# Kernel optimization log

Measured on AMD Instinct MI355X. Metric: run time of the kernel, lower is better.

The kernel has to match this reference:

```python
import jax, jax.numpy as jnp
import numpy as np
from jax import lax

B, L = 8, 128
V, P = 30000, 50
EMB, POS = 300, 30
H = 256            # rnn_hidden per direction
H2 = 2 * H         # BiLSTM output dim
NBIO, NLAB = 9, 10
ROUNDS = 2
IN = EMB + POS
NEG = -100000000000.0


def setup_inputs() -> dict:
    key = jax.random.key(0)
    ks = jax.random.split(key, 25)
    tokens = jax.random.randint(ks[0], (B, L), 1, V)
    pos = jax.random.randint(ks[1], (B, L), 1, P)
    lens = jax.random.randint(ks[2], (B,), L // 2, L + 1)
    mask_s = (jnp.arange(L)[None, :] < lens[:, None]).astype(jnp.float32)

    def g(k, shape, s=0.05):
        return jax.random.normal(k, shape, dtype=jnp.float32) * s

    return dict(
        tokens=tokens, pos=pos, mask_s=mask_s,
        emb=g(ks[3], (V, EMB), 0.5), pos_emb=g(ks[4], (P, POS), 0.5),
        Wih_f=g(ks[5], (4 * H, IN)), Whh_f=g(ks[6], (4 * H, H)), b_f=g(ks[7], (4 * H,)),
        Wih_b=g(ks[8], (4 * H, IN)), Whh_b=g(ks[9], (4 * H, H)), b_b=g(ks[10], (4 * H,)),
        Wg_ih=g(ks[11], (3 * H2, NBIO)), Wg_hh=g(ks[12], (3 * H2, H2)),
        bg_ih=g(ks[13], (3 * H2,)), bg_hh=g(ks[14], (3 * H2,)),
        Wr_ih=g(ks[15], (3 * H2, NLAB)), Wr_hh=g(ks[16], (3 * H2, H2)),
        br_ih=g(ks[17], (3 * H2,)), br_hh=g(ks[18], (3 * H2,)),
        W_Lr=g(ks[19], (H2, 2 * H2)), b_Lr=g(ks[20], (H2,)),
        W_Cr=g(ks[21], (NLAB, H2)), b_Cr=g(ks[22], (NLAB,)),
        W_Cg=g(ks[23], (NBIO, H2)), b_Cg=g(ks[24], (NBIO,)),
    )


def lstm_dir(x, m, Wih, Whh, b, reverse):
    # x: [B,L,IN], m: [B,L]. Masked updates emulate pack_padded_sequence
    # (state held at padded steps; padded outputs zeroed by caller).
    Bn = x.shape[0]
    h0 = jnp.zeros((Bn, H), x.dtype)
    c0 = jnp.zeros((Bn, H), x.dtype)

    def step(carry, inp):
        h, c = carry
        xt, mt = inp  # [B,IN], [B,1]
        gates = xt @ Wih.T + h @ Whh.T + b
        i, f, g, o = jnp.split(gates, 4, axis=-1)
        i = jax.nn.sigmoid(i); f = jax.nn.sigmoid(f)
        g = jnp.tanh(g); o = jax.nn.sigmoid(o)
        c_new = f * c + i * g
        h_new = o * jnp.tanh(c_new)
        h = mt * h_new + (1.0 - mt) * h
        c = mt * c_new + (1.0 - mt) * c
        return (h, c), h

    xs = (jnp.swapaxes(x, 0, 1), m.T[:, :, None])
    _, hs = lax.scan(step, (h0, c0), xs, reverse=reverse)
    return jnp.swapaxes(hs, 0, 1)  # [B,L,H]


def gru_cell(x, h, Wih, Whh, bih, bhh):
    gi = x @ Wih.T + bih
    gh = h @ Whh.T + bhh
    ir, iz, inn = jnp.split(gi, 3, axis=-1)
    hr, hz, hn = jnp.split(gh, 3, axis=-1)
    r = jax.nn.sigmoid(ir + hr)
    z = jax.nn.sigmoid(iz + hz)
    n = jnp.tanh(inn + r * hn)
    return (1.0 - z) * n + z * h


def pair_scores(Hr, W_Lr, b_Lr, W_Cr, b_Cr):
    # Lr([e1;e2]) split: e12 @ W_Lr.T = e1 @ W1.T + e2 @ W2.T (avoids 4H concat)
    W1, W2 = W_Lr[:, :H2], W_Lr[:, H2:]
    a = jnp.einsum('blh,oh->blo', Hr, W1)  # [B,L,H2]
    b2 = jnp.einsum('blh,oh->blo', Hr, W2)
    e = jax.nn.relu(a[:, :, None, :] + b2[:, None, :, :] + b_Lr)  # [B,L,L,H2]
    return jax.nn.sigmoid(jnp.einsum('bsth,kh->bstk', e, W_Cr) + b_Cr)  # [B,L,L,NLAB]


def reference(tokens, pos, mask_s, emb, pos_emb,
              Wih_f, Whh_f, b_f, Wih_b, Whh_b, b_b,
              Wg_ih, Wg_hh, bg_ih, bg_hh,
              Wr_ih, Wr_hh, br_ih, br_hh,
              W_Lr, b_Lr, W_Cr, b_Cr, W_Cg, b_Cg):
    x = jnp.concatenate([emb[tokens], pos_emb[pos]], axis=2)  # [B,L,IN]
    hf = lstm_dir(x, mask_s, Wih_f, Whh_f, b_f, reverse=False)
    hb = lstm_dir(x, mask_s, Wih_b, Whh_b, b_b, reverse=True)
    Henc = jnp.concatenate([hf, hb], axis=2) * mask_s[:, :, None]  # [B,L,H2]

    m2 = mask_s[:, :, None] * mask_s[:, None, :]  # [B,L,L] pair mask
    m3 = m2[:, :, :, None]                        # [B,L,L,1]

    Hc, Hg, Hr = Henc, Henc, Henc
    for _ in range(ROUNDS):
        prob_Cg = jax.nn.softmax(Hg @ W_Cg.T + b_Cg, axis=2)        # [B,L,NBIO]
        prob_Cr = pair_scores(Hr, W_Lr, b_Lr, W_Cr, b_Cr)            # [B,L,L,NLAB]
        prob_Cr = jnp.where(m3 > 0, prob_Cr, NEG)
        prob_Cr = prob_Cr.max(axis=2)                                # [B,L,NLAB]
        hflat = Hc.reshape(-1, H2)
        Hg = gru_cell(prob_Cg.reshape(-1, NBIO), hflat, Wg_ih, Wg_hh, bg_ih, bg_hh).reshape(Hc.shape)
        Hr = gru_cell(prob_Cr.reshape(-1, NLAB), hflat, Wr_ih, Wr_hh, br_ih, br_hh).reshape(Hc.shape)
        Hc = Hc + Hr + Hg

    logits_Cg = jax.nn.log_softmax(Hg @ W_Cg.T + b_Cg, axis=2) * mask_s[:, :, None]
    logits_Cr = pair_scores(Hr, W_Lr, b_Lr, W_Cr, b_Cr) * m3
    return logits_Cg, logits_Cr
```

## Files before the change

### kernel.cpp

```cpp
#include <hip/hip_runtime.h>
#include <hip/hip_bf16.h>
#include <stdint.h>

#define DEVI __device__ __forceinline__

static constexpr int Bn = 8, Ln = 128;
static constexpr int EMBc = 300, POSc = 30, INc = 330;
static constexpr int KPAD = 384;
static constexpr int Hc = 256, H2c = 512, G4 = 1024, G3 = 1536;
static constexpr int G2 = 2048;
static constexpr int GHW = 3072;
static constexpr int NBIOc = 9, NLABc = 10;
static constexpr float NEGc = -100000000000.0f;

typedef __attribute__((ext_vector_type(8))) short bf16x8;
typedef __attribute__((ext_vector_type(4))) float f32x4;

DEVI float sigf(float x) { return 1.0f / (1.0f + __expf(-x)); }

DEVI unsigned short b16rne(float f) {
    union { float f; unsigned u; } v; v.f = f;
    unsigned u = v.u;
    return (unsigned short)((u + 0x7FFFu + ((u >> 16) & 1u)) >> 16);
}

__global__ void k_prep0(const int* __restrict__ tok, const int* __restrict__ pos,
                        const float* __restrict__ emb, const float* __restrict__ pemb,
                        const float* __restrict__ WihF, const float* __restrict__ WihB,
                        const float* __restrict__ bF, const float* __restrict__ bB,
                        ushort* __restrict__ x, ushort* __restrict__ WihFB,
                        float* __restrict__ biasFB, uint32_t* __restrict__ hG32) {
    int i = blockIdx.x * 256 + threadIdx.x;
    const int N0 = Bn * Ln * KPAD;
    const int N1 = N0 + G2 * KPAD;
    const int N2 = N1 + G2;
    const int N3 = N2 + 8192;
    if (i < N0) {
        int bl = i / KPAD, c = i - bl * KPAD;
        float v = 0.f;
        if (c < EMBc) v = emb[tok[bl] * EMBc + c];
        else if (c < INc) v = pemb[pos[bl] * POSc + (c - EMBc)];
        x[i] = b16rne(v);
    } else if (i < N1) {
        int w = i - N0;
        int r = w / KPAD, c = w - r * KPAD;
        float v = 0.f;
        if (c < INc) v = (r < G4) ? WihF[(size_t)r * INc + c] : WihB[(size_t)(r - G4) * INc + c];
        WihFB[w] = b16rne(v);
    } else if (i < N2) {
        int j = i - N1;
        biasFB[j] = (j < G4) ? bF[j] : bB[j - G4];
    } else if (i < N3) {
        __hip_atomic_store(&hG32[i - N2], 0u, __ATOMIC_RELAXED, __HIP_MEMORY_SCOPE_AGENT);
    }
}

DEVI void gemm_tile(const ushort* __restrict__ A, const ushort* __restrict__ B,
                    const float* __restrict__ bias, float* __restrict__ C,
                    int N, int K, int m0, int n0,
                    ushort (*As)[72], ushort (*Bs)[72]) {
    int tid = threadIdx.x;
    int lane = tid & 63, wv = tid >> 6;
    int mw = (wv >> 1) * 32, nw = (wv & 1) * 32;
    int lr16 = lane & 15, g4 = lane >> 4;
    f32x4 acc[2][2] = {};
    for (int k0 = 0; k0 < K; k0 += 64) {
#pragma unroll
        for (int it = 0; it < 2; it++) {
            int idx = tid + it * 256;
            int r = idx >> 3, ch = idx & 7;
            uint4 av = *(const uint4*)(A + (size_t)(m0 + r) * K + k0 + ch * 8);
            *(uint4*)(&As[r][ch * 8]) = av;
            uint4 bv2 = *(const uint4*)(B + (size_t)(n0 + r) * K + k0 + ch * 8);
            *(uint4*)(&Bs[r][ch * 8]) = bv2;
        }
        __syncthreads();
#pragma unroll
        for (int ks = 0; ks < 2; ks++) {
            bf16x8 af[2], bfr[2];
#pragma unroll
            for (int i = 0; i < 2; i++) {
                af[i]  = *(const bf16x8*)(&As[mw + i * 16 + lr16][ks * 32 + g4 * 8]);
                bfr[i] = *(const bf16x8*)(&Bs[nw + i * 16 + lr16][ks * 32 + g4 * 8]);
            }
#pragma unroll
            for (int i = 0; i < 2; i++)
#pragma unroll
                for (int j = 0; j < 2; j++)
                    acc[i][j] = __builtin_amdgcn_mfma_f32_16x16x32_bf16(af[i], bfr[j], acc[i][j], 0, 0, 0);
        }
        __syncthreads();
    }
#pragma unroll
    for (int i = 0; i < 2; i++)
#pragma unroll
        for (int j = 0; j < 2; j++)
#pragma unroll
            for (int r2 = 0; r2 < 4; r2++) {
                int mm = m0 + mw + i * 16 + g4 * 4 + r2;
                int nn = n0 + nw + j * 16 + lr16;
                C[(size_t)mm * N + nn] = acc[i][j][r2] + (bias ? bias[nn] : 0.f);
            }
}

__global__ __launch_bounds__(256) void k_xproj(
    const ushort* __restrict__ x_bf, const ushort* __restrict__ WihFB,
    const float* __restrict__ biasFB, float* __restrict__ Xpre,
    const float* __restrict__ Wg_hh, const float* __restrict__ Wr_hh,
    const float* __restrict__ W_Lr, const float* __restrict__ bg_hh,
    const float* __restrict__ br_hh,
    const float* __restrict__ Wg_ih, const float* __restrict__ Wr_ih,
    ushort* __restrict__ WhhGR, ushort* __restrict__ WLrAB, float* __restrict__ biasGR,
    float* __restrict__ WgihT, float* __restrict__ WrihT) {
    int bid = blockIdx.x;
    __shared__ __align__(16) ushort As[64][72];
    __shared__ __align__(16) ushort Bs[64][72];
    if (bid < 512) {
        int nt = bid & 31, mt = bid >> 5;
        gemm_tile(x_bf, WihFB, biasFB, Xpre, G2, KPAD, mt * 64, nt * 64, As, Bs);
        return;
    }
    const int stride = 128 * 256;
    int pid = (bid - 512) * 256 + threadIdx.x;
    for (int idx = pid; idx < GHW * H2c; idx += stride) {
        int r = idx >> 9, c = idx & 511;
        float v = (r < G3) ? Wg_hh[(size_t)r * H2c + c] : Wr_hh[(size_t)(r - G3) * H2c + c];
        WhhGR[idx] = b16rne(v);
    }
    for (int idx = pid; idx < G4 * H2c; idx += stride) {
        int r = idx >> 9, c = idx & 511;
        float v = (r < H2c) ? W_Lr[(size_t)r * (2 * H2c) + c]
                            : W_Lr[(size_t)(r - H2c) * (2 * H2c) + H2c + c];
        WLrAB[idx] = b16rne(v);
    }
    for (int idx = pid; idx < GHW; idx += stride)
        biasGR[idx] = (idx < G3) ? bg_hh[idx] : br_hh[idx - G3];
    for (int idx = pid; idx < NBIOc * G3; idx += stride) {
        int k = idx / G3, rj = idx - k * G3;
        WgihT[idx] = Wg_ih[(size_t)rj * NBIOc + k];
    }
    for (int idx = pid; idx < NLABc * G3; idx += stride) {
        int k = idx / G3, rj = idx - k * G3;
        WrihT[idx] = Wr_ih[(size_t)rj * NLABc + k];
    }
}

__global__ __launch_bounds__(512) void k_lstm_mfma(
    const float* __restrict__ Xpre, const float* __restrict__ WhhF,
    const float* __restrict__ WhhB, const float* __restrict__ mask,
    float* __restrict__ Henc, ushort* __restrict__ HencB,
    unsigned long long* __restrict__ hG) {
    const int blk = blockIdx.x;
    const int d = blk >> 2, q = blk & 3;
    const float* Whh = d ? WhhB : WhhF;
    const int tid = threadIdx.x;
    const int lane = tid & 63, wv = tid >> 6;
    const int lr16 = lane & 15, g4 = lane >> 4;

    __shared__ __align__(16) uint32_t hlds[2][8 * 136];
    __shared__ float Glds[256][9];

    bf16x8 aw[16];
#pragma unroll
    for (int jt2 = 0; jt2 < 2; jt2++) {
        int jt = wv * 2 + jt2;
        int lr = jt * 16 + lr16;
        int g = lr >> 6, jj = lr & 63;
        int R = g * 256 + q * 64 + jj;
        const float* wr = Whh + (size_t)R * 256;
#pragma unroll
        for (int kt = 0; kt < 8; kt++) {
            int k0 = kt * 32 + g4 * 8;
            float4 f0 = *(const float4*)(wr + k0);
            float4 f1 = *(const float4*)(wr + k0 + 4);
            bf16x8 a;
            a[0] = (short)b16rne(f0.x); a[1] = (short)b16rne(f0.y);
            a[2] = (short)b16rne(f0.z); a[3] = (short)b16rne(f0.w);
            a[4] = (short)b16rne(f1.x); a[5] = (short)b16rne(f1.y);
            a[6] = (short)b16rne(f1.z); a[7] = (short)b16rne(f1.w);
            aw[jt2 * 8 + kt] = a;
        }
    }

    const int jj_t = tid & 63, b_t = tid >> 6;
    float hval = 0.f, cval = 0.f;
    const int bcol = lane & 15;
    const int bb = lane & 7;
    const int u1 = tid + 512;

    for (int s = 0; s < Ln; s++) {
        const int t = d ? (Ln - 1 - s) : s;

        const float* xrow = Xpre + ((size_t)(b_t * Ln + t)) * G2 + d * G4 + q * 64 + jj_t;
        float xg0 = xrow[0], xg1 = xrow[256], xg2 = xrow[512], xg3 = xrow[768];
        float mval = mask[b_t * Ln + t];

        const unsigned long long* slot = hG + ((size_t)(s & 1) * 2 + d) * 1024;
        unsigned long long ea, eb;
        do {
            ea = __hip_atomic_load(slot + tid, __ATOMIC_RELAXED, __HIP_MEMORY_SCOPE_AGENT);
            eb = __hip_atomic_load(slot + u1,  __ATOMIC_RELAXED, __HIP_MEMORY_SCOPE_AGENT);
        } while ((unsigned)(ea >> 32) != (unsigned)s || (unsigned)(eb >> 32) != (unsigned)s);
        uint32_t* hb = hlds[s & 1];
        hb[(tid >> 7) * 136 + (tid & 127)] = (uint32_t)ea;
        hb[(u1 >> 7) * 136 + (u1 & 127)]  = (uint32_t)eb;
        __syncthreads();

        bf16x8 bv[8];
#pragma unroll
        for (int kt = 0; kt < 8; kt++)
            bv[kt] = *(const bf16x8*)(&hb[bb * 136 + kt * 16 + g4 * 4]);

        f32x4 acc0 = {0.f, 0.f, 0.f, 0.f}, acc1 = {0.f, 0.f, 0.f, 0.f};
#pragma unroll
        for (int kt = 0; kt < 8; kt++) {
            acc0 = __builtin_amdgcn_mfma_f32_16x16x32_bf16(aw[kt], bv[kt], acc0, 0, 0, 0);
            acc1 = __builtin_amdgcn_mfma_f32_16x16x32_bf16(aw[8 + kt], bv[kt], acc1, 0, 0, 0);
        }

        if (bcol < 8) {
            int lrb0 = (wv * 2 + 0) * 16 + g4 * 4;
            int lrb1 = (wv * 2 + 1) * 16 + g4 * 4;
#pragma unroll
            for (int r2 = 0; r2 < 4; r2++) Glds[lrb0 + r2][bcol] = acc0[r2];
#pragma unroll
            for (int r2 = 0; r2 < 4; r2++) Glds[lrb1 + r2][bcol] = acc1[r2];
        }
        __syncthreads();

        float iv = sigf(xg0 + Glds[jj_t][b_t]);
        float fv = sigf(xg1 + Glds[64 + jj_t][b_t]);
        float gv = tanhf(xg2 + Glds[128 + jj_t][b_t]);
        float ov = sigf(xg3 + Glds[192 + jj_t][b_t]);
        float cn = fv * cval + iv * gv;
        float hn = ov * tanhf(cn);
        float hv = mval * hn + (1.f - mval) * hval;
        cval = mval * cn + (1.f - mval) * cval;
        hval = hv;

        int hbits = (int)b16rne(hv);
        int pbits = __shfl_xor(hbits, 1);
        if ((jj_t & 1) == 0) {
            uint32_t dataw = ((uint32_t)hbits & 0xFFFFu) | ((uint32_t)pbits << 16);
            unsigned long long word = ((unsigned long long)(unsigned)(s + 1) << 32) | dataw;
            __hip_atomic_store(hG + ((size_t)((s + 1) & 1) * 2 + d) * 1024 +
                                   b_t * 128 + q * 32 + (jj_t >> 1),
                               word, __ATOMIC_RELAXED, __HIP_MEMORY_SCOPE_AGENT);
        }
        float ho = hv * mval;
        size_t hidx = ((size_t)(b_t * Ln + t)) * H2c + d * Hc + q * 64 + jj_t;
        Henc[hidx] = ho;
        HencB[hidx] = b16rne(ho);
        __syncthreads();
    }
}

__global__ __launch_bounds__(256) void k_mega(
    int nGh,
    const ushort* __restrict__ Agh, const ushort* __restrict__ Bgh,
    const float* __restrict__ biasGh, float* __restrict__ Cgh,
    const ushort* __restrict__ Apc, const ushort* __restrict__ Bpc,
    float* __restrict__ Cpc,
    const float* __restrict__ Hp9, const float* __restrict__ W9,
    const float* __restrict__ b9, float* __restrict__ out9) {
    int bid = blockIdx.x;
    __shared__ __align__(16) ushort As[64][72];
    __shared__ __align__(16) ushort Bs[64][72];
    if (bid < nGh) {
        int nt = bid % 48, mt = bid / 48;
        gemm_tile(Agh, Bgh, biasGh, Cgh, GHW, H2c, mt * 64, nt * 64, As, Bs);
    } else if (bid < nGh + 256) {
        int b2 = bid - nGh;
        int nt = b2 & 15, mt = b2 >> 4;
        gemm_tile(Apc, Bpc, nullptr, Cpc, G4, H2c, mt * 64, nt * 64, As, Bs);
    } else {
        int b3 = bid - nGh - 256;
        int lane = threadIdx.x & 63, wvv = threadIdx.x >> 6;
        int row = b3 * 4 + wvv;
        const float4* h4 = (const float4*)(Hp9 + (size_t)row * H2c + lane * 8);
        float4 h0 = h4[0], h1 = h4[1];
        float acc[NBIOc];
#pragma unroll
        for (int k = 0; k < NBIOc; k++) {
            const float4* w4 = (const float4*)(W9 + (size_t)k * H2c + lane * 8);
            float4 w0 = w4[0], w1 = w4[1];
            acc[k] = h0.x * w0.x + h0.y * w0.y + h0.z * w0.z + h0.w * w0.w +
                     h1.x * w1.x + h1.y * w1.y + h1.z * w1.z + h1.w * w1.w;
        }
#pragma unroll
        for (int off = 32; off >= 1; off >>= 1)
#pragma unroll
            for (int k = 0; k < NBIOc; k++) acc[k] += __shfl_down(acc[k], off);
        if (lane == 0) {
#pragma unroll
            for (int k = 0; k < NBIOc; k++) out9[(size_t)row * NBIOc + k] = acc[k] + b9[k];
        }
    }
}

__global__ __launch_bounds__(128) void k_pairgru(
    const float* __restrict__ Cp, const float* __restrict__ bL,
    const float* __restrict__ WCr, const float* __restrict__ bCr,
    const float* __restrict__ mask, const float* __restrict__ cg,
    const float* __restrict__ gh,
    const float* __restrict__ WgihT, const float* __restrict__ bg_ih,
    const float* __restrict__ WrihT, const float* __restrict__ br_ih,
    const float* __restrict__ hprev,
    float* __restrict__ Hg_out, float* __restrict__ Hcb_out,
    ushort* __restrict__ Hrb_out, ushort* __restrict__ Hcbb_out) {
    int m = blockIdx.x;
    int b = m >> 7;
    __shared__ __align__(16) float As[H2c];
    __shared__ __align__(16) float Ws[NLABc][H2c];
    __shared__ float red[NLABc][128];
    __shared__ float pCr_s[NLABc];
    int tid = threadIdx.x;
    for (int i = tid; i < H2c; i += 128) As[i] = Cp[(size_t)m * G4 + i] + bL[i];
    for (int i = tid; i < NLABc * H2c; i += 128) Ws[i / H2c][i % H2c] = WCr[i];
    __syncthreads();
    {
        int t = tid;
        float m3 = mask[m] * mask[b * Ln + t];
        float outv[NLABc];
        if (m3 > 0.f) {
            float4 acc[NLABc];
#pragma unroll
            for (int k = 0; k < NLABc; k++) acc[k] = make_float4(0.f, 0.f, 0.f, 0.f);
            const float4* B4 = (const float4*)(Cp + (size_t)(b * Ln + t) * G4 + H2c);
            const float4* A4 = (const float4*)As;
            for (int qq = 0; qq < H2c / 4; qq++) {
                float4 a = A4[qq], bb = B4[qq];
                float4 e;
                e.x = fmaxf(a.x + bb.x, 0.f);
                e.y = fmaxf(a.y + bb.y, 0.f);
                e.z = fmaxf(a.z + bb.z, 0.f);
                e.w = fmaxf(a.w + bb.w, 0.f);
#pragma unroll
                for (int k = 0; k < NLABc; k++) {
                    float4 w = *(const float4*)(&Ws[k][qq * 4]);
                    acc[k].x += e.x * w.x; acc[k].y += e.y * w.y;
                    acc[k].z += e.z * w.z; acc[k].w += e.w * w.w;
                }
            }
#pragma unroll
            for (int k = 0; k < NLABc; k++)
                outv[k] = sigf(acc[k].x + acc[k].y + acc[k].z + acc[k].w + bCr[k]);
        } else {
#pragma unroll
            for (int k = 0; k < NLABc; k++) outv[k] = NEGc;
        }
#pragma unroll
        for (int k = 0; k < NLABc; k++) red[k][tid] = outv[k];
    }
    __syncthreads();
    for (int off = 64; off >= 1; off >>= 1) {
        if (tid < off) {
#pragma unroll
            for (int k = 0; k < NLABc; k++) red[k][tid] = fmaxf(red[k][tid], red[k][tid + off]);
        }
        __syncthreads();
    }
    if (tid < NLABc) pCr_s[tid] = red[tid][0];
    __syncthreads();

    float v[NBIOc], mx = -3.4e38f;
#pragma unroll
    for (int k = 0; k < NBIOc; k++) { v[k] = cg[m * NBIOc + k]; mx = fmaxf(mx, v[k]); }
    float ssum = 0.f;
#pragma unroll
    for (int k = 0; k < NBIOc; k++) { v[k] = __expf(v[k] - mx); ssum += v[k]; }
    float inv = 1.f / ssum;
#pragma unroll
    for (int k = 0; k < NBIOc; k++) v[k] *= inv;

    const float* g1b = gh + (size_t)m * GHW;
#pragma unroll
    for (int u = 0; u < 4; u++) {
        int j = tid + u * 128;
        size_t i = (size_t)m * H2c + j;

        float gr = bg_ih[j], gz = bg_ih[H2c + j], gn = bg_ih[2 * H2c + j];
#pragma unroll
        for (int k = 0; k < NBIOc; k++) {
            float pv = v[k];
            gr += WgihT[k * G3 + j] * pv;
            gz += WgihT[k * G3 + H2c + j] * pv;
            gn += WgihT[k * G3 + 2 * H2c + j] * pv;
        }
        float hp = hprev[i];
        float r1 = sigf(gr + g1b[j]);
        float z1 = sigf(gz + g1b[H2c + j]);
        float n1 = tanhf(gn + r1 * g1b[2 * H2c + j]);
        float hg = (1.f - z1) * n1 + z1 * hp;

        float rr = br_ih[j], rz = br_ih[H2c + j], rn = br_ih[2 * H2c + j];
#pragma unroll
        for (int k = 0; k < NLABc; k++) {
            float pv = pCr_s[k];
            rr += WrihT[k * G3 + j] * pv;
            rz += WrihT[k * G3 + H2c + j] * pv;
            rn += WrihT[k * G3 + 2 * H2c + j] * pv;
        }
        const float* g2b = g1b + G3;
        float r2 = sigf(rr + g2b[j]);
        float z2 = sigf(rz + g2b[H2c + j]);
        float n2 = tanhf(rn + r2 * g2b[2 * H2c + j]);
        float hr = (1.f - z2) * n2 + z2 * hp;

        float hc = hp + hr + hg;
        Hg_out[i] = hg;
        Hcb_out[i] = hc;
        Hrb_out[i] = b16rne(hr);
        Hcbb_out[i] = b16rne(hc);
    }
}

__global__ __launch_bounds__(128) void k_final_out(
    const float* __restrict__ Cp, const float* __restrict__ bL,
    const float* __restrict__ WCr, const float* __restrict__ bCr,
    const float* __restrict__ mask, const float* __restrict__ cg,
    float* __restrict__ outp) {
    int bid = blockIdx.x;
    int tid = threadIdx.x;
    if (bid >= Bn * Ln) {
        int r = (bid - Bn * Ln) * 128 + tid;
        float v[NBIOc], mx = -3.4e38f;
#pragma unroll
        for (int k = 0; k < NBIOc; k++) { v[k] = cg[r * NBIOc + k]; mx = fmaxf(mx, v[k]); }
        float s = 0.f;
#pragma unroll
        for (int k = 0; k < NBIOc; k++) s += __expf(v[k] - mx);
        float lse = mx + __logf(s);
        float m = mask[r];
#pragma unroll
        for (int k = 0; k < NBIOc; k++) outp[r * NBIOc + k] = (v[k] - lse) * m;
        return;
    }
    int bs = bid;
    int b = bs >> 7;
    __shared__ __align__(16) float As[H2c];
    __shared__ __align__(16) float Ws[NLABc][H2c];
    for (int i = tid; i < H2c; i += 128) As[i] = Cp[(size_t)bs * G4 + i] + bL[i];
    for (int i = tid; i < NLABc * H2c; i += 128) Ws[i / H2c][i % H2c] = WCr[i];
    __syncthreads();
    int t = tid;
    float m3 = mask[bs] * mask[b * Ln + t];
    float outv[NLABc];
    if (m3 > 0.f) {
        float4 acc[NLABc];
#pragma unroll
        for (int k = 0; k < NLABc; k++) acc[k] = make_float4(0.f, 0.f, 0.f, 0.f);
        const float4* B4 = (const float4*)(Cp + (size_t)(b * Ln + t) * G4 + H2c);
        const float4* A4 = (const float4*)As;
        for (int qq = 0; qq < H2c / 4; qq++) {
            float4 a = A4[qq], bb = B4[qq];
            float4 e;
            e.x = fmaxf(a.x + bb.x, 0.f);
            e.y = fmaxf(a.y + bb.y, 0.f);
            e.z = fmaxf(a.z + bb.z, 0.f);
            e.w = fmaxf(a.w + bb.w, 0.f);
#pragma unroll
            for (int k = 0; k < NLABc; k++) {
                float4 w = *(const float4*)(&Ws[k][qq * 4]);
                acc[k].x += e.x * w.x; acc[k].y += e.y * w.y;
                acc[k].z += e.z * w.z; acc[k].w += e.w * w.w;
            }
        }
#pragma unroll
        for (int k = 0; k < NLABc; k++)
            outv[k] = sigf(acc[k].x + acc[k].y + acc[k].z + acc[k].w + bCr[k]);
    } else {
#pragma unroll
        for (int k = 0; k < NLABc; k++) outv[k] = 0.f;
    }
    size_t base = (size_t)(Bn * Ln * NBIOc) + ((size_t)bs * Ln + t) * NLABc;
#pragma unroll
    for (int k = 0; k < NLABc; k++) outp[base + k] = outv[k];
}

extern "C" void kernel_launch(void* const* d_in, const int* in_sizes, int n_in,
                              void* d_out, int out_size, void* d_ws, size_t ws_size,
                              hipStream_t stream) {
    const int*   tok   = (const int*)d_in[0];
    const int*   pos   = (const int*)d_in[1];
    const float* mask  = (const float*)d_in[2];
    const float* emb   = (const float*)d_in[3];
    const float* pemb  = (const float*)d_in[4];
    const float* WihF  = (const float*)d_in[5];
    const float* WhhF  = (const float*)d_in[6];
    const float* bF    = (const float*)d_in[7];
    const float* WihB  = (const float*)d_in[8];
    const float* WhhB  = (const float*)d_in[9];
    const float* bB    = (const float*)d_in[10];
    const float* Wg_ih = (const float*)d_in[11];
    const float* Wg_hh = (const float*)d_in[12];
    const float* bg_ih = (const float*)d_in[13];
    const float* bg_hh = (const float*)d_in[14];
    const float* Wr_ih = (const float*)d_in[15];
    const float* Wr_hh = (const float*)d_in[16];
    const float* br_ih = (const float*)d_in[17];
    const float* br_hh = (const float*)d_in[18];
    const float* W_Lr  = (const float*)d_in[19];
    const float* b_Lr  = (const float*)d_in[20];
    const float* W_Cr  = (const float*)d_in[21];
    const float* b_Cr  = (const float*)d_in[22];
    const float* W_Cg  = (const float*)d_in[23];
    const float* b_Cg  = (const float*)d_in[24];

    float* outp = (float*)d_out;
    float* ws = (float*)d_ws;

    unsigned long long* hG = (unsigned long long*)ws;
    size_t off = 8192;
    auto alloc = [&](size_t n) { off = (off + 3) & ~(size_t)3; float* p = ws + off; off += n; return p; };
    auto allocU = [&](size_t n_us) { off = (off + 3) & ~(size_t)3; ushort* p = (ushort*)(ws + off); off += (n_us + 1) / 2; return p; };

    float* R1 = alloc((size_t)G4 * GHW);
    float* Xpre = R1;
    float* gh   = R1;
    ushort* WihFB_bf = (ushort*)(R1 + (size_t)G4 * G2);
    ushort* x_bf     = (ushort*)(R1 + (size_t)G4 * G2 + 393216);
    float*  biasFB   = R1 + (size_t)G4 * G2 + 393216 + 196608;

    float*  pairC    = alloc((size_t)G4 * G4);
    ushort* WhhGR_bf = allocU((size_t)GHW * H2c);
    ushort* WLrAB_bf = allocU((size_t)G4 * H2c);
    float*  biasGR   = alloc(GHW);
    float*  WgihT    = alloc((size_t)NBIOc * G3);
    float*  WrihT    = alloc((size_t)NLABc * G3);
    float*  Henc     = alloc((size_t)Bn * Ln * H2c);
    ushort* Henc_bf  = allocU((size_t)Bn * Ln * H2c);
    float*  Hg       = alloc((size_t)Bn * Ln * H2c);
    float*  Hcb      = alloc((size_t)Bn * Ln * H2c);
    ushort* Hr_bf    = allocU((size_t)Bn * Ln * H2c);
    ushort* Hcb_bf   = allocU((size_t)Bn * Ln * H2c);
    float*  cg       = alloc((size_t)Bn * Ln * NBIOc);
    (void)ws_size; (void)in_sizes; (void)n_in; (void)out_size;

    {
        int total = Bn * Ln * KPAD + G2 * KPAD + G2 + 8192;
        k_prep0<<<(total + 255) / 256, 256, 0, stream>>>(
            tok, pos, emb, pemb, WihF, WihB, bF, bB, x_bf, WihFB_bf, biasFB,
            (uint32_t*)hG);
    }

    k_xproj<<<640, 256, 0, stream>>>(x_bf, WihFB_bf, biasFB, Xpre,
                                     Wg_hh, Wr_hh, W_Lr, bg_hh, br_hh,
                                     Wg_ih, Wr_ih,
                                     WhhGR_bf, WLrAB_bf, biasGR, WgihT, WrihT);

    k_lstm_mfma<<<8, 512, 0, stream>>>(Xpre, WhhF, WhhB, mask, Henc, Henc_bf, hG);

    const float*  Hgs    = Henc;
    const ushort* Hrs_bf = Henc_bf;
    const float*  Hcs    = Henc;
    const ushort* Hcs_bf = Henc_bf;
    for (int r = 0; r < 2; r++) {
        k_mega<<<768 + 512, 256, 0, stream>>>(768,
            Hcs_bf, WhhGR_bf, biasGR, gh,
            Hrs_bf, WLrAB_bf, pairC,
            Hgs, W_Cg, b_Cg, cg);
        k_pairgru<<<Bn * Ln, 128, 0, stream>>>(
            pairC, b_Lr, W_Cr, b_Cr, mask, cg, gh,
            WgihT, bg_ih, WrihT, br_ih, Hcs,
            Hg, Hcb, Hr_bf, Hcb_bf);
        Hgs = Hg; Hrs_bf = Hr_bf; Hcs = Hcb; Hcs_bf = Hcb_bf;
    }

    k_mega<<<512, 256, 0, stream>>>(0,
        nullptr, nullptr, nullptr, nullptr,
        Hrs_bf, WLrAB_bf, pairC,
        Hgs, W_Cg, b_Cg, cg);
    k_final_out<<<Bn * Ln + 8, 128, 0, stream>>>(pairC, b_Lr, W_Cr, b_Cr, mask, cg, outp);
}
```

Measured before the change: 399.3 us.

## Split LSTM recurrence across two blocks per direction to cut cross-block sync

The recurrent LSTM kernel now runs 4 blocks of 1024 threads instead of 8 blocks of 512, so each direction is split across 2 blocks, each owning 128 hidden units. Each block writes its own half of h straight into LDS and only polls global memory for the partner block's half. This is meant to shrink the per-step inter-block spin-wait and global traffic on the serial critical path. In exchange each block runs more waves and register-resident weights, which may reduce occupancy, and the LDS gate buffer doubles.

```diff
diff --git a/kernel.cpp b/kernel.cpp
--- a/kernel.cpp
+++ b/kernel.cpp
@@ -145,28 +145,27 @@
     }
 }
 
-__global__ __launch_bounds__(512) void k_lstm_mfma(
+__global__ __launch_bounds__(1024) void k_lstm_mfma(
     const float* __restrict__ Xpre, const float* __restrict__ WhhF,
     const float* __restrict__ WhhB, const float* __restrict__ mask,
     float* __restrict__ Henc, ushort* __restrict__ HencB,
     unsigned long long* __restrict__ hG) {
     const int blk = blockIdx.x;
-    const int d = blk >> 2, q = blk & 3;
+    const int d = blk >> 1, q2 = blk & 1, qp = q2 ^ 1;
     const float* Whh = d ? WhhB : WhhF;
     const int tid = threadIdx.x;
     const int lane = tid & 63, wv = tid >> 6;
     const int lr16 = lane & 15, g4 = lane >> 4;
 
     __shared__ __align__(16) uint32_t hlds[2][8 * 136];
-    __shared__ float Glds[256][9];
+    __shared__ float Glds[512][9];
 
     bf16x8 aw[16];
 #pragma unroll
     for (int jt2 = 0; jt2 < 2; jt2++) {
-        int jt = wv * 2 + jt2;
-        int lr = jt * 16 + lr16;
-        int g = lr >> 6, jj = lr & 63;
-        int R = g * 256 + q * 64 + jj;
+        int L = (wv * 2 + jt2) * 16 + lr16;
+        int g = L >> 7, jjL = L & 127;
+        int R = g * 256 + q2 * 128 + jjL;
         const float* wr = Whh + (size_t)R * 256;
 #pragma unroll
         for (int kt = 0; kt < 8; kt++) {
@@ -182,28 +181,33 @@
         }
     }
 
-    const int jj_t = tid & 63, b_t = tid >> 6;
+    const int jj_t = tid & 127, b_t = tid >> 7;
     float hval = 0.f, cval = 0.f;
     const int bcol = lane & 15;
     const int bb = lane & 7;
-    const int u1 = tid + 512;
+
+    for (int i = tid; i < 8 * 136; i += 1024) hlds[0][i] = 0u;
+    __syncthreads();
+
+    const int pb = tid >> 6, pp = tid & 63;
 
     for (int s = 0; s < Ln; s++) {
         const int t = d ? (Ln - 1 - s) : s;
 
-        const float* xrow = Xpre + ((size_t)(b_t * Ln + t)) * G2 + d * G4 + q * 64 + jj_t;
+        const float* xrow = Xpre + ((size_t)(b_t * Ln + t)) * G2 + d * G4 + q2 * 128 + jj_t;
         float xg0 = xrow[0], xg1 = xrow[256], xg2 = xrow[512], xg3 = xrow[768];
         float mval = mask[b_t * Ln + t];
 
-        const unsigned long long* slot = hG + ((size_t)(s & 1) * 2 + d) * 1024;
-        unsigned long long ea, eb;
-        do {
-            ea = __hip_atomic_load(slot + tid, __ATOMIC_RELAXED, __HIP_MEMORY_SCOPE_AGENT);
-            eb = __hip_atomic_load(slot + u1,  __ATOMIC_RELAXED, __HIP_MEMORY_SCOPE_AGENT);
-        } while ((unsigned)(ea >> 32) != (unsigned)s || (unsigned)(eb >> 32) != (unsigned)s);
         uint32_t* hb = hlds[s & 1];
-        hb[(tid >> 7) * 136 + (tid & 127)] = (uint32_t)ea;
-        hb[(u1 >> 7) * 136 + (u1 & 127)]  = (uint32_t)eb;
+        if (tid < 512) {
+            const unsigned long long* slot = hG + ((size_t)(s & 1) * 2 + d) * 1024;
+            unsigned long long e;
+            do {
+                e = __hip_atomic_load(slot + pb * 128 + qp * 64 + pp,
+                                      __ATOMIC_RELAXED, __HIP_MEMORY_SCOPE_AGENT);
+            } while ((unsigned)(e >> 32) != (unsigned)s);
+            hb[pb * 136 + qp * 64 + pp] = (uint32_t)e;
+        }
         __syncthreads();
 
         bf16x8 bv[8];
@@ -229,9 +233,9 @@
         __syncthreads();
 
         float iv = sigf(xg0 + Glds[jj_t][b_t]);
-        float fv = sigf(xg1 + Glds[64 + jj_t][b_t]);
-        float gv = tanhf(xg2 + Glds[128 + jj_t][b_t]);
-        float ov = sigf(xg3 + Glds[192 + jj_t][b_t]);
+        float fv = sigf(xg1 + Glds[128 + jj_t][b_t]);
+        float gv = tanhf(xg2 + Glds[256 + jj_t][b_t]);
+        float ov = sigf(xg3 + Glds[384 + jj_t][b_t]);
         float cn = fv * cval + iv * gv;
         float hn = ov * tanhf(cn);
         float hv = mval * hn + (1.f - mval) * hval;
@@ -244,11 +248,12 @@
             uint32_t dataw = ((uint32_t)hbits & 0xFFFFu) | ((uint32_t)pbits << 16);
             unsigned long long word = ((unsigned long long)(unsigned)(s + 1) << 32) | dataw;
             __hip_atomic_store(hG + ((size_t)((s + 1) & 1) * 2 + d) * 1024 +
-                                   b_t * 128 + q * 32 + (jj_t >> 1),
+                                   b_t * 128 + q2 * 64 + (jj_t >> 1),
                                word, __ATOMIC_RELAXED, __HIP_MEMORY_SCOPE_AGENT);
+            hlds[(s + 1) & 1][b_t * 136 + q2 * 64 + (jj_t >> 1)] = dataw;
         }
         float ho = hv * mval;
-        size_t hidx = ((size_t)(b_t * Ln + t)) * H2c + d * Hc + q * 64 + jj_t;
+        size_t hidx = ((size_t)(b_t * Ln + t)) * H2c + d * Hc + q2 * 128 + jj_t;
         Henc[hidx] = ho;
         HencB[hidx] = b16rne(ho);
         __syncthreads();
@@ -549,7 +554,7 @@
                                      Wg_ih, Wr_ih,
                                      WhhGR_bf, WLrAB_bf, biasGR, WgihT, WrihT);
 
-    k_lstm_mfma<<<8, 512, 0, stream>>>(Xpre, WhhF, WhhB, mask, Henc, Henc_bf, hG);
+    k_lstm_mfma<<<4, 1024, 0, stream>>>(Xpre, WhhF, WhhB, mask, Henc, Henc_bf, hG);
 
     const float*  Hgs    = Henc;
     const ushort* Hrs_bf = Henc_bf;
```

Result: slower. 501.4 us (+25.6%).
